# Performance work log

Measured on AMD Instinct MI355X. Metric: run time of the kernel, lower is better.

## Reference

```python
import jax, jax.numpy as jnp
import numpy as np

DIM = 2048
N_HEADS = 16
HEAD_DIM = DIM // N_HEADS
ROPE_BASE = 10000.0


def _rope_cos_sin(seq_len, head_dim, dtype):
    inv_freq = 1.0 / (ROPE_BASE ** (jnp.arange(0, head_dim, 2, dtype=jnp.float32) / head_dim))
    t = jnp.arange(seq_len, dtype=jnp.float32)
    freqs = jnp.einsum('s,d->sd', t, inv_freq)          # (S, hd/2)
    emb = jnp.concatenate([freqs, freqs], axis=-1)       # (S, hd)
    return jnp.cos(emb).astype(dtype), jnp.sin(emb).astype(dtype)


def _rotate_half(x):
    x1, x2 = jnp.split(x, 2, axis=-1)
    return jnp.concatenate([-x2, x1], axis=-1)


def _apply_rope(x, cos, sin):
    # x: (B, H, S, hd); cos/sin: (S, hd)
    return x * cos[None, None] + _rotate_half(x) * sin[None, None]


def setup_inputs() -> dict:
    key = jax.random.key(0)
    ks = jax.random.split(key, 5)
    B, S = 2, 2048
    scale = 1.0 / np.sqrt(DIM)
    return {
        'x': jax.random.normal(ks[0], (B, S, DIM), dtype=jnp.float32),
        'Wq': jax.random.normal(ks[1], (DIM, DIM), dtype=jnp.float32) * scale,
        'Wk': jax.random.normal(ks[2], (DIM, DIM), dtype=jnp.float32) * scale,
        'Wv': jax.random.normal(ks[3], (DIM, DIM), dtype=jnp.float32) * scale,
        'Wo': jax.random.normal(ks[4], (DIM, DIM), dtype=jnp.float32) * scale,
    }


def reference(x, Wq, Wk, Wv, Wo):
    B, S, _ = x.shape
    scale = HEAD_DIM ** -0.5

    def proj(W):
        # torch Linear: x @ W.T ; reshape to (B, H, S, hd)
        return (x @ W.T).reshape(B, S, N_HEADS, HEAD_DIM).transpose(0, 2, 1, 3)

    q, k, v = proj(Wq), proj(Wk), proj(Wv)
    cos, sin = _rope_cos_sin(S, HEAD_DIM, x.dtype)
    q = _apply_rope(q, cos, sin)
    k = _apply_rope(k, cos, sin)

    scores = jnp.einsum('bhqd,bhkd->bhqk', q, k) * scale  # (B,H,S,S)
    causal = jnp.triu(jnp.ones((S, S), dtype=bool), k=1)
    scores = jnp.where(causal[None, None], -jnp.inf, scores)
    attn = jax.nn.softmax(scores.astype(jnp.float32), axis=-1).astype(q.dtype)
    out = jnp.einsum('bhqk,bhkd->bhqd', attn, v)          # (B,H,S,hd)
    out = out.transpose(0, 2, 1, 3).reshape(B, S, DIM)
    return out @ Wo.T
```

## Files before the change

kernel.cpp:

```cpp
#include <hip/hip_runtime.h>


#define SEQ 2048
#define DMODEL 2048
#define NH 16
#define HD 128

typedef __attribute__((ext_vector_type(8))) short bf16x8;
typedef __attribute__((ext_vector_type(4))) float f32x4;

__device__ __forceinline__ unsigned short f2bf(float f) {
  unsigned int u = __float_as_uint(f);
  u += 0x7fffu + ((u >> 16) & 1u);
  return (unsigned short)(u >> 16);
}

__device__ __forceinline__ void g2l16(const void* g, void* l) {
  __builtin_amdgcn_global_load_lds((const __attribute__((address_space(1))) void*)g,
                                   (__attribute__((address_space(3))) void*)l,
                                   16, 0, 0);
}

__device__ __forceinline__ f32x4 mfma16(bf16x8 a, bf16x8 b, f32x4 c) {
  return __builtin_amdgcn_mfma_f32_16x16x32_bf16(a, b, c, 0, 0, 0);
}

template <int CTRL>
__device__ __forceinline__ float dpp_ror(float v) {
  return __int_as_float(__builtin_amdgcn_mov_dpp(__float_as_int(v), CTRL, 0xf, 0xf, false));
}
__device__ __forceinline__ float red_max16(float v) {
  v = fmaxf(v, dpp_ror<0x128>(v));
  v = fmaxf(v, dpp_ror<0x124>(v));
  v = fmaxf(v, dpp_ror<0x122>(v));
  v = fmaxf(v, dpp_ror<0x121>(v));
  return v;
}
__device__ __forceinline__ float red_sum16(float v) {
  v += dpp_ror<0x128>(v);
  v += dpp_ror<0x124>(v);
  v += dpp_ror<0x122>(v);
  v += dpp_ror<0x121>(v);
  return v;
}

__global__ __launch_bounds__(256) void cvt_all(const float* __restrict__ x,
                                               const float* __restrict__ wq,
                                               const float* __restrict__ wk,
                                               const float* __restrict__ wv,
                                               const float* __restrict__ wo,
                                               unsigned short* __restrict__ dst0,
                                               float2* __restrict__ rtab) {
  const int b = blockIdx.x;
  if (b >= 24576) {
    const int idx = (b - 24576) * 256 + threadIdx.x;
    const int s = idx >> 6, d = idx & 63;
    float sn, cs;
    sincosf((float)s * exp2f(-0.20762050593046f * (float)d), &sn, &cs);
    rtab[idx] = make_float2(cs, sn);
    return;
  }
  const float* src;
  unsigned short* dst;
  int idx, r = -1;
  if (b < 8192) {
    src = x; dst = dst0; idx = b * 256 + threadIdx.x;
  } else {
    r = (b - 8192) >> 12;
    src = (r == 0) ? wq : (r == 1) ? wk : (r == 2) ? wv : wo;
    dst = dst0 + (size_t)2 * SEQ * DMODEL + (size_t)r * DMODEL * DMODEL;
    idx = ((b - 8192) & 4095) * 256 + threadIdx.x;
  }
  const float4 v = ((const float4*)src)[idx];
  ushort4 o;
  o.x = f2bf(v.x); o.y = f2bf(v.y); o.z = f2bf(v.z); o.w = f2bf(v.w);
  int widx = idx;
  if (r == 0 || r == 1) {
    const int row = idx >> 9, col = idx & 511;
    const int o_ = row & 127;
    const int e = (((o_ >> 4) & 3) << 5) | (((o_ >> 6) & 1) << 4) | (o_ & 15);
    widx = (((row & ~127) | e) << 9) | col;
  }
  ((ushort4*)dst)[widx] = o;
}

template <int MODE>
__global__ __launch_bounds__(512, 2) void gemm_pipe(
    const unsigned short* __restrict__ A,
    const unsigned short* __restrict__ B,
    unsigned short* __restrict__ obf,
    float* __restrict__ of32,
    const float2* __restrict__ rtab) {
  __shared__ unsigned short lds[3 * 24576];
  const int nb = blockIdx.x, mb = blockIdx.y;
  const int M0 = mb * 256;
  const int t = threadIdx.x;
  const int w = t >> 6, lane = t & 63, l15 = lane & 15, quad = lane >> 4;
  const int g = lane >> 3, j = lane & 7;
  const int wm = w >> 1, wn = w & 1;

  const unsigned short* Abase = A + (size_t)M0 * DMODEL;
  const unsigned short* Bbase = B + (size_t)nb * 128 * DMODEL;

  f32x4 acc[4][4] = {};

  auto stage = [&](int buf, int k0, int i0) {
#pragma unroll
    for (int i = 0; i < 3; ++i) {
      const int u = w * 6 + i0 + i;
      if (u < 32) {
        const int row = u * 8 + g;
        g2l16(Abase + (size_t)row * DMODEL + k0 + ((j ^ g) << 3),
              &lds[buf * 24576 + u * 512]);
      } else {
        const int row = (u - 32) * 8 + g;
        g2l16(Bbase + (size_t)row * DMODEL + k0 + ((j ^ g) << 3),
              &lds[buf * 24576 + 16384 + (u - 32) * 512]);
      }
    }
  };

  auto comp = [&](int buf, int kc) {
    const int c = kc * 4 + quad;
    const unsigned short* As_ = &lds[buf * 24576];
    const unsigned short* Bs_ = &lds[buf * 24576 + 16384];
    bf16x8 af[4], bf[4];
#pragma unroll
    for (int mt = 0; mt < 4; ++mt) {
      const int m = wm * 64 + mt * 16 + l15;
      af[mt] = *(const bf16x8*)&As_[m * 64 + ((c ^ (m & 7)) << 3)];
    }
#pragma unroll
    for (int nt = 0; nt < 4; ++nt) {
      const int n = wn * 64 + nt * 16 + l15;
      bf[nt] = *(const bf16x8*)&Bs_[n * 64 + ((c ^ (n & 7)) << 3)];
    }
#pragma unroll
    for (int nt = 0; nt < 4; ++nt)
#pragma unroll
      for (int mt = 0; mt < 4; ++mt)
        acc[mt][nt] = mfma16(af[mt], bf[nt], acc[mt][nt]);
  };

  stage(0, 0, 0);
  stage(0, 0, 3);
  stage(1, 64, 0);
  stage(1, 64, 3);
  asm volatile("s_waitcnt vmcnt(6)\n\ts_barrier" ::: "memory");

  int buf = 0, b2 = 2;
  for (int tt = 0; tt < 32; ++tt) {
    const int k0 = tt * 64;
    if (tt < 30) stage(b2, k0 + 128, 0);
    comp(buf, 0);
    if (tt < 30) stage(b2, k0 + 128, 3);
    comp(buf, 1);
    if (tt < 30) {
      asm volatile("s_waitcnt vmcnt(6)\n\ts_barrier" ::: "memory");
    } else if (tt == 30) {
      asm volatile("s_waitcnt vmcnt(0)\n\ts_barrier" ::: "memory");
    }
    buf = (buf == 2) ? 0 : buf + 1;
    b2 = (b2 == 2) ? 0 : b2 + 1;
  }

  if (MODE == 0) {
    const size_t NX = (size_t)2 * SEQ * DMODEL;
    const int z = nb >> 4;
    const int h = nb & 15;
    if (z < 2) {
      const float qscale = (z == 0) ? 0.1275174356f : 1.0f;
      unsigned short* O = obf + (size_t)z * NX;
#pragma unroll
      for (int mt = 0; mt < 4; ++mt)
#pragma unroll
        for (int reg = 0; reg < 4; ++reg) {
          const int m = M0 + wm * 64 + mt * 16 + quad * 4 + reg;
          const int bb = m >> 11, s = m & 2047;
          unsigned short* ob = O + ((size_t)(bb * NH + h) * SEQ + s) * HD;
#pragma unroll
          for (int p = 0; p < 2; ++p) {
            const int q = wn * 2 + p;
            const float2 cs = rtab[s * 64 + q * 16 + l15];
            const float x1 = acc[mt][2 * p][reg], x2 = acc[mt][2 * p + 1][reg];
            ob[wn * 64 + (2 * p) * 16 + l15] = f2bf((x1 * cs.x - x2 * cs.y) * qscale);
            ob[wn * 64 + (2 * p + 1) * 16 + l15] = f2bf((x2 * cs.x + x1 * cs.y) * qscale);
          }
        }
    } else {
      unsigned short* Vb = obf + 2 * NX + (size_t)h * HD * SEQ;
#pragma unroll
      for (int mt = 0; mt < 4; ++mt)
#pragma unroll
        for (int reg = 0; reg < 4; ++reg) {
          const int m = M0 + wm * 64 + mt * 16 + quad * 4 + reg;
          const int bb = m >> 11, s = m & 2047;
          unsigned short* ob = Vb + (size_t)bb * NH * HD * SEQ;
#pragma unroll
          for (int nt = 0; nt < 4; ++nt)
            ob[(size_t)(wn * 64 + nt * 16 + l15) * SEQ + s] = f2bf(acc[mt][nt][reg]);
        }
    }
  } else {
#pragma unroll
    for (int mt = 0; mt < 4; ++mt)
#pragma unroll
      for (int reg = 0; reg < 4; ++reg) {
        const int m = M0 + wm * 64 + mt * 16 + quad * 4 + reg;
#pragma unroll
        for (int nt = 0; nt < 4; ++nt)
          of32[(size_t)m * DMODEL + nb * 128 + wn * 64 + nt * 16 + l15] =
              acc[mt][nt][reg];
      }
  }
}

__global__ __launch_bounds__(256) void attn_kernel(const unsigned short* __restrict__ Q,
                                                   const unsigned short* __restrict__ K,
                                                   const unsigned short* __restrict__ Vt,
                                                   unsigned short* __restrict__ Oa) {
  __shared__ unsigned short Ks[256 * 64];
  __shared__ unsigned short Vs[256 * 64];
  const int gid = blockIdx.x;
  const int bh = gid & 31;
  const int pr = gid >> 5;
  const unsigned short* Qb = Q + (size_t)bh * SEQ * HD;
  const unsigned short* Kb = K + (size_t)bh * SEQ * HD;
  const unsigned short* Vb = Vt + (size_t)bh * HD * SEQ;
  const int t = threadIdx.x;
  const int w = t >> 6, lane = t & 63, l15 = lane & 15, quad = lane >> 4;
  const int g = lane >> 3, j = lane & 7;
  const int b = bh >> 4, h = bh & 15;
  const int r2r = l15 ^ ((l15 >> 2) & 2);

  for (int half = 0; half < 2; ++half) {
    const int qt = half ? 31 - pr : pr;
    const int ktmax = (qt * 64 + 63) >> 7;

    bf16x8 qf[4];
#pragma unroll
    for (int ch = 0; ch < 4; ++ch)
      qf[ch] = *(const bf16x8*)(Qb + (size_t)(qt * 64 + w * 16 + l15) * HD +
                                ch * 32 + quad * 8);

    f32x4 o[8] = {};
    float mrow[4], lrow[4];
#pragma unroll
    for (int reg = 0; reg < 4; ++reg) { mrow[reg] = -1e30f; lrow[reg] = 0.f; }

    for (int kt = 0; kt <= ktmax; ++kt) {
      __syncthreads();
#pragma unroll
      for (int r = 0; r < 16; ++r) {
        const int u = r * 4 + w;
        if (u < 32) {
          const int vrow = u * 8 + g, key = vrow >> 1;
          const int ck = j ^ (key & 7);
          g2l16(Kb + (size_t)(kt * 128 + key) * HD + (vrow & 1) * 64 + ck * 8, &Ks[u * 512]);
        } else {
          const int u2 = u - 32;
          const int vrow = u2 * 8 + g, d = vrow >> 1;
          const int cv = j ^ (d & 7);
          g2l16(Vb + (size_t)d * SEQ + kt * 128 + (vrow & 1) * 64 + cv * 8, &Vs[u2 * 512]);
        }
      }
      __syncthreads();

      const bool halftile = (kt == ktmax) && !(qt & 1);
      f32x4 s[8] = {};
      __builtin_amdgcn_s_setprio(1);
#pragma unroll
      for (int ch = 0; ch < 4; ++ch) {
        const int hh = ch >> 1, c = (ch & 1) * 4 + quad;
#pragma unroll
        for (int nt = 0; nt < 4; ++nt) {
          const int n = nt * 16 + l15;
          const bf16x8 bv = *(const bf16x8*)&Ks[(n * 2 + hh) * 64 + ((c ^ (n & 7)) << 3)];
          s[nt] = mfma16(qf[ch], bv, s[nt]);
        }
      }
      if (!halftile) {
#pragma unroll
        for (int ch = 0; ch < 4; ++ch) {
          const int hh = ch >> 1, c = (ch & 1) * 4 + quad;
#pragma unroll
          for (int nt = 4; nt < 8; ++nt) {
            const int n = nt * 16 + l15;
            const bf16x8 bv = *(const bf16x8*)&Ks[(n * 2 + hh) * 64 + ((c ^ (n & 7)) << 3)];
            s[nt] = mfma16(qf[ch], bv, s[nt]);
          }
        }
      }
      __builtin_amdgcn_s_setprio(0);

      if (kt == ktmax) {
#pragma unroll
        for (int nt = 0; nt < 8; ++nt)
#pragma unroll
          for (int reg = 0; reg < 4; ++reg) {
            const int rr = qt * 64 + w * 16 + quad * 4 + reg;
            const int cc = kt * 128 + nt * 16 + l15;
            if (cc > rr) s[nt][reg] = -1e30f;
          }
      }

#pragma unroll
      for (int reg = 0; reg < 4; ++reg) {
        float vmax = s[0][reg];
#pragma unroll
        for (int nt = 1; nt < 8; ++nt) vmax = fmaxf(vmax, s[nt][reg]);
        vmax = red_max16(vmax);
        const float mo = mrow[reg];
        float mn = mo;
        if (!__all(vmax <= mo + 8.0f)) {
          mn = fmaxf(mo, vmax);
          const float alpha = exp2f(mo - mn);
          mrow[reg] = mn;
          lrow[reg] *= alpha;
#pragma unroll
          for (int nt = 0; nt < 8; ++nt) o[nt][reg] *= alpha;
        }
        float rs = 0.f;
#pragma unroll
        for (int nt = 0; nt < 8; ++nt) {
          const float p_ = exp2f(s[nt][reg] - mn);
          s[nt][reg] = p_;
          rs += p_;
        }
        rs = red_sum16(rs);
        lrow[reg] += rs;
      }

      __syncthreads();

      unsigned short* Pw = &Ks[w * 2048];
#pragma unroll
      for (int nt = 0; nt < 8; ++nt)
#pragma unroll
        for (int reg = 0; reg < 4; ++reg) {
          const int r2 = quad * 4 + (reg ^ (quad & 2));
          const int key = nt * 16 + l15;
          Pw[(key >> 3) * 128 + r2 * 8 + (key & 7)] = f2bf(s[nt][reg]);
        }

      __builtin_amdgcn_s_setprio(1);
#pragma unroll
      for (int ch = 0; ch < 4; ++ch) {
        const int kh = ch >> 1, c = (ch & 1) * 4 + quad;
        const bf16x8 pa = *(const bf16x8*)&Pw[(ch * 4 + quad) * 128 + r2r * 8];
#pragma unroll
        for (int nt = 0; nt < 8; ++nt) {
          const int d = nt * 16 + l15;
          const bf16x8 vv = *(const bf16x8*)&Vs[(d * 2 + kh) * 64 + ((c ^ (d & 7)) << 3)];
          o[nt] = mfma16(pa, vv, o[nt]);
        }
      }
      __builtin_amdgcn_s_setprio(0);
    }

#pragma unroll
    for (int reg = 0; reg < 4; ++reg) {
      const int sq = qt * 64 + w * 16 + quad * 4 + reg;
      const float inv_l = 1.0f / lrow[reg];
      unsigned short* ob = Oa + (size_t)(b * SEQ + sq) * DMODEL + h * HD;
#pragma unroll
      for (int nt = 0; nt < 8; ++nt) ob[nt * 16 + l15] = f2bf(o[nt][reg] * inv_l);
    }
  }
}

extern "C" void kernel_launch(void* const* d_in, const int* in_sizes, int n_in,
                              void* d_out, int out_size, void* d_ws, size_t ws_size,
                              hipStream_t stream) {
  const float* x = (const float*)d_in[0];
  const float* Wq = (const float*)d_in[1];
  const float* Wk = (const float*)d_in[2];
  const float* Wv = (const float*)d_in[3];
  const float* Wo = (const float*)d_in[4];
  float* out = (float*)d_out;

  const size_t NX = (size_t)2 * SEQ * DMODEL;
  const size_t NW = (size_t)DMODEL * DMODEL;
  unsigned short* ws = (unsigned short*)d_ws;
  unsigned short* xb = ws;
  unsigned short* wqb = xb + NX;
  unsigned short* wkb = wqb + NW;
  unsigned short* wvb = wkb + NW;
  unsigned short* wob = wvb + NW;
  unsigned short* qb = wob + NW;
  unsigned short* kb = qb + NX;
  unsigned short* vb = kb + NX;
  unsigned short* ab = vb + NX;
  float2* rtab = (float2*)(ab + NX);

  cvt_all<<<25088, 256, 0, stream>>>(x, Wq, Wk, Wv, Wo, ws, rtab);
  gemm_pipe<0><<<dim3(48, 16), 512, 0, stream>>>(xb, wqb, qb, nullptr, rtab);
  attn_kernel<<<512, 256, 0, stream>>>(qb, kb, vb, ab);
  gemm_pipe<1><<<dim3(16, 16), 512, 0, stream>>>(ab, wob, nullptr, out, nullptr);
}
```

Baseline: 412.7 us.

## Double-buffer K/V tiles with 64-key blocks and per-wave causal skipping

The attention kernel now uses 64-key tiles instead of 128 and double-buffers K and V in LDS. The load of the next tile is issued before computing the current one, so global loads overlap with MFMA work, and there is one barrier per iteration. P moves to its own per-wave LDS buffer instead of reusing the K buffer, which drops a sync. On the diagonal tile, each wave computes only the key subtiles its causal mask needs. The cost is more LDS per block, which may lower occupancy, twice as many loop iterations, and no XOR swizzle on the P writes, which may cause bank conflicts.

```diff
diff --git a/kernel.cpp b/kernel.cpp
--- a/kernel.cpp
+++ b/kernel.cpp
@@ -219,8 +219,9 @@
                                                    const unsigned short* __restrict__ K,
                                                    const unsigned short* __restrict__ Vt,
                                                    unsigned short* __restrict__ Oa) {
-  __shared__ unsigned short Ks[256 * 64];
-  __shared__ unsigned short Vs[256 * 64];
+  __shared__ unsigned short Ks[2][64 * 128];
+  __shared__ unsigned short Vs[2][128 * 64];
+  __shared__ unsigned short Ps[4][1024];
   const int gid = blockIdx.x;
   const int bh = gid & 31;
   const int pr = gid >> 5;
@@ -229,13 +230,31 @@
   const unsigned short* Vb = Vt + (size_t)bh * HD * SEQ;
   const int t = threadIdx.x;
   const int w = t >> 6, lane = t & 63, l15 = lane & 15, quad = lane >> 4;
-  const int g = lane >> 3, j = lane & 7;
+  const int l7 = lane & 7;
   const int b = bh >> 4, h = bh & 15;
-  const int r2r = l15 ^ ((l15 >> 2) & 2);
+  const int uA = w * 64 + lane;
+
+  auto stage = [&](int sb, int kt) {
+    const unsigned short* Kt = Kb + (size_t)(kt * 64) * HD;
+    const unsigned short* Vtk = Vb + kt * 64;
+#pragma unroll
+    for (int i = 0; i < 4; ++i) {
+      const int u = i * 256 + uA;
+      const int key = u >> 4, cs = u & 15;
+      g2l16(Kt + (size_t)key * HD + ((cs ^ (key & 7)) << 3),
+            &Ks[sb][(i * 256 + w * 64) * 8]);
+    }
+#pragma unroll
+    for (int i = 0; i < 4; ++i) {
+      const int u = i * 256 + uA;
+      const int d = u >> 3, cs = u & 7;
+      g2l16(Vtk + (size_t)d * SEQ + ((cs ^ (d & 7)) << 3),
+            &Vs[sb][(i * 256 + w * 64) * 8]);
+    }
+  };
 
   for (int half = 0; half < 2; ++half) {
     const int qt = half ? 31 - pr : pr;
-    const int ktmax = (qt * 64 + 63) >> 7;
 
     bf16x8 qf[4];
 #pragma unroll
@@ -248,58 +267,38 @@
 #pragma unroll
     for (int reg = 0; reg < 4; ++reg) { mrow[reg] = -1e30f; lrow[reg] = 0.f; }
 
-    for (int kt = 0; kt <= ktmax; ++kt) {
-      __syncthreads();
-#pragma unroll
-      for (int r = 0; r < 16; ++r) {
-        const int u = r * 4 + w;
-        if (u < 32) {
-          const int vrow = u * 8 + g, key = vrow >> 1;
-          const int ck = j ^ (key & 7);
-          g2l16(Kb + (size_t)(kt * 128 + key) * HD + (vrow & 1) * 64 + ck * 8, &Ks[u * 512]);
-        } else {
-          const int u2 = u - 32;
-          const int vrow = u2 * 8 + g, d = vrow >> 1;
-          const int cv = j ^ (d & 7);
-          g2l16(Vb + (size_t)d * SEQ + kt * 128 + (vrow & 1) * 64 + cv * 8, &Vs[u2 * 512]);
-        }
-      }
-      __syncthreads();
-
-      const bool halftile = (kt == ktmax) && !(qt & 1);
-      f32x4 s[8] = {};
+    stage(0, 0);
+    asm volatile("s_waitcnt vmcnt(0)\n\ts_barrier" ::: "memory");
+    int buf = 0;
+
+    for (int kt = 0; kt <= qt; ++kt) {
+      if (kt < qt) stage(buf ^ 1, kt + 1);
+
+      const bool diag = (kt == qt);
+      const int ntm = diag ? w : 3;
+      f32x4 s[4] = {};
       __builtin_amdgcn_s_setprio(1);
 #pragma unroll
       for (int ch = 0; ch < 4; ++ch) {
-        const int hh = ch >> 1, c = (ch & 1) * 4 + quad;
+        const int c = ch * 4 + quad;
 #pragma unroll
         for (int nt = 0; nt < 4; ++nt) {
-          const int n = nt * 16 + l15;
-          const bf16x8 bv = *(const bf16x8*)&Ks[(n * 2 + hh) * 64 + ((c ^ (n & 7)) << 3)];
-          s[nt] = mfma16(qf[ch], bv, s[nt]);
-        }
-      }
-      if (!halftile) {
-#pragma unroll
-        for (int ch = 0; ch < 4; ++ch) {
-          const int hh = ch >> 1, c = (ch & 1) * 4 + quad;
-#pragma unroll
-          for (int nt = 4; nt < 8; ++nt) {
+          if (nt <= ntm) {
             const int n = nt * 16 + l15;
-            const bf16x8 bv = *(const bf16x8*)&Ks[(n * 2 + hh) * 64 + ((c ^ (n & 7)) << 3)];
+            const bf16x8 bv = *(const bf16x8*)&Ks[buf][n * 128 + ((c ^ l7) << 3)];
             s[nt] = mfma16(qf[ch], bv, s[nt]);
           }
         }
       }
       __builtin_amdgcn_s_setprio(0);
 
-      if (kt == ktmax) {
-#pragma unroll
-        for (int nt = 0; nt < 8; ++nt)
+      if (diag) {
+#pragma unroll
+        for (int nt = 0; nt < 4; ++nt)
 #pragma unroll
           for (int reg = 0; reg < 4; ++reg) {
-            const int rr = qt * 64 + w * 16 + quad * 4 + reg;
-            const int cc = kt * 128 + nt * 16 + l15;
+            const int rr = w * 16 + quad * 4 + reg;
+            const int cc = nt * 16 + l15;
             if (cc > rr) s[nt][reg] = -1e30f;
           }
       }
@@ -308,7 +307,7 @@
       for (int reg = 0; reg < 4; ++reg) {
         float vmax = s[0][reg];
 #pragma unroll
-        for (int nt = 1; nt < 8; ++nt) vmax = fmaxf(vmax, s[nt][reg]);
+        for (int nt = 1; nt < 4; ++nt) vmax = fmaxf(vmax, s[nt][reg]);
         vmax = red_max16(vmax);
         const float mo = mrow[reg];
         float mn = mo;
@@ -322,7 +321,7 @@
         }
         float rs = 0.f;
 #pragma unroll
-        for (int nt = 0; nt < 8; ++nt) {
+        for (int nt = 0; nt < 4; ++nt) {
           const float p_ = exp2f(s[nt][reg] - mn);
           s[nt][reg] = p_;
           rs += p_;
@@ -331,31 +330,31 @@
         lrow[reg] += rs;
       }
 
-      __syncthreads();
-
-      unsigned short* Pw = &Ks[w * 2048];
-#pragma unroll
-      for (int nt = 0; nt < 8; ++nt)
+      unsigned short* Pw = Ps[w];
+#pragma unroll
+      for (int nt = 0; nt < 4; ++nt)
 #pragma unroll
         for (int reg = 0; reg < 4; ++reg) {
-          const int r2 = quad * 4 + (reg ^ (quad & 2));
           const int key = nt * 16 + l15;
-          Pw[(key >> 3) * 128 + r2 * 8 + (key & 7)] = f2bf(s[nt][reg]);
+          Pw[(key >> 3) * 128 + (quad * 4 + reg) * 8 + (key & 7)] = f2bf(s[nt][reg]);
         }
 
       __builtin_amdgcn_s_setprio(1);
 #pragma unroll
-      for (int ch = 0; ch < 4; ++ch) {
-        const int kh = ch >> 1, c = (ch & 1) * 4 + quad;
-        const bf16x8 pa = *(const bf16x8*)&Pw[(ch * 4 + quad) * 128 + r2r * 8];
+      for (int ch2 = 0; ch2 < 2; ++ch2) {
+        const int c = ch2 * 4 + quad;
+        const bf16x8 pa = *(const bf16x8*)&Pw[c * 128 + l15 * 8];
 #pragma unroll
         for (int nt = 0; nt < 8; ++nt) {
           const int d = nt * 16 + l15;
-          const bf16x8 vv = *(const bf16x8*)&Vs[(d * 2 + kh) * 64 + ((c ^ (d & 7)) << 3)];
+          const bf16x8 vv = *(const bf16x8*)&Vs[buf][d * 64 + ((c ^ l7) << 3)];
           o[nt] = mfma16(pa, vv, o[nt]);
         }
       }
       __builtin_amdgcn_s_setprio(0);
+
+      asm volatile("s_waitcnt vmcnt(0)\n\ts_barrier" ::: "memory");
+      buf ^= 1;
     }
 
 #pragma unroll
```

Measured after the change: 377.1 us. -8.6%, faster.
